# Optimization experiments

Hardware: AMD Instinct MI355X
Metric: run time of the kernel (lower is better)

The kernel has to match this reference:

```python
import jax, jax.numpy as jnp
import numpy as np

EPS = 1e-4

def _mp_normalize(x):
    # EDM2-style normalize: divide by (eps + RMS-scaled L2 norm) along last dim -> unit RMS
    n = jnp.linalg.norm(x, axis=-1, keepdims=True)
    n = EPS + n * (1.0 / np.sqrt(x.shape[-1]))
    return x / n

def _mp_linear(x, w):
    # magnitude-preserving linear: row-normalized weight scaled by 1/sqrt(fan_in), no bias
    fan_in = w.shape[-1]
    w_hat = _mp_normalize(w) * (1.0 / np.sqrt(fan_in))
    return x @ w_hat.T

def setup_inputs() -> dict:
    key = jax.random.key(0)
    k1, k2, k3 = jax.random.split(key, 3)
    B, T, D = 2, 2048, 1024
    x = jax.random.normal(k1, (B, T, D), dtype=jnp.float32)
    w_qkv = jax.random.normal(k2, (3 * D, D), dtype=jnp.float32)
    w_out = jax.random.normal(k3, (D, D), dtype=jnp.float32)
    return {"x": x, "w_qkv": w_qkv, "w_out": w_out}

def reference(x, w_qkv, w_out):
    B, T, D = x.shape
    H = 16
    hd = D // H
    scale = 1.0 / np.sqrt(hd)

    qkv = _mp_linear(x, w_qkv)                      # (B, T, 3D)
    q, k, v = jnp.split(qkv, 3, axis=-1)            # each (B, T, D)

    def to_heads(t):
        return t.reshape(B, T, H, hd).transpose(0, 2, 1, 3)  # (B, H, T, hd)

    q, k, v = to_heads(q), to_heads(k), to_heads(v)
    q = _mp_normalize(q)
    k = _mp_normalize(k)

    scores = jnp.einsum("bhqd,bhkd->bhqk", q, k) * scale
    attn = jax.nn.softmax(scores, axis=-1)
    out = jnp.einsum("bhqk,bhkd->bhqd", attn, v)    # (B, H, T, hd)
    out = out.transpose(0, 2, 1, 3).reshape(B, T, D)
    return _mp_linear(out, w_out)
```

## Files before the change

kernel.cpp:

```cpp
#include <hip/hip_runtime.h>

#define BATCH  2
#define SEQ    2048
#define DMODEL 1024
#define NHEAD  16
#define HDIM   64
#define NROWS  (BATCH * SEQ)
#define QKVC   (3 * DMODEL)

typedef float f32x4 __attribute__((ext_vector_type(4)));
typedef float f32x16 __attribute__((ext_vector_type(16)));
typedef short s16x8 __attribute__((ext_vector_type(8)));
typedef short s16x4 __attribute__((ext_vector_type(4)));
typedef unsigned int u32x4 __attribute__((ext_vector_type(4)));

__device__ __forceinline__ unsigned short f2bf(float f) {
  unsigned int u = __float_as_uint(f);
  u = (u + 0x7FFFu + ((u >> 16) & 1u)) >> 16;
  return (unsigned short)u;
}
__device__ __forceinline__ float bf2f(unsigned short s) {
  return __uint_as_float(((unsigned int)s) << 16);
}
__device__ __forceinline__ unsigned pkbf(float a, float b) {
  unsigned r;
  asm("v_cvt_pk_bf16_f32 %0, %1, %2" : "=v"(r) : "v"(a), "v"(b));
  return r;
}
__device__ __forceinline__ void swp(unsigned &a, unsigned &b) {
  asm volatile("v_permlane32_swap_b32 %0, %1" : "+v"(a), "+v"(b));
}

__global__ __launch_bounds__(256) void k_wnorm(const float* __restrict__ Wq_src,
                                               const float* __restrict__ Wo_src,
                                               unsigned short* __restrict__ Wq,
                                               unsigned short* __restrict__ Wo) {
  const int row = blockIdx.x, tid = threadIdx.x;
  const float* src = (row < QKVC) ? (Wq_src + (size_t)row * DMODEL)
                                  : (Wo_src + (size_t)(row - QKVC) * DMODEL);
  unsigned short* dst = (row < QKVC) ? (Wq + (size_t)row * DMODEL)
                                     : (Wo + (size_t)(row - QKVC) * DMODEL);
  float4 v = ((const float4*)src)[tid];
  float ss = v.x * v.x + v.y * v.y + v.z * v.z + v.w * v.w;
#pragma unroll
  for (int m = 1; m < 64; m <<= 1) ss += __shfl_xor(ss, m);
  __shared__ float part[4];
  if ((tid & 63) == 0) part[tid >> 6] = ss;
  __syncthreads();
  const float tot = part[0] + part[1] + part[2] + part[3];
  const float scale = 0.03125f / (1e-4f + sqrtf(tot) * 0.03125f);
  unsigned short* op = dst + tid * 4;
  op[0] = f2bf(v.x * scale); op[1] = f2bf(v.y * scale);
  op[2] = f2bf(v.z * scale); op[3] = f2bf(v.w * scale);
}

__global__ __launch_bounds__(256) void k_cast(const float* __restrict__ X,
                                              unsigned short* __restrict__ Xb) {
  const int i = blockIdx.x * 256 + threadIdx.x;
  const float4 v = ((const float4*)X)[i];
  ushort4 o = { f2bf(v.x), f2bf(v.y), f2bf(v.z), f2bf(v.w) };
  ((ushort4*)Xb)[i] = o;
}

#define LDP 88
__global__ __launch_bounds__(256, 3) void k_gemm_qkv(const unsigned short* __restrict__ A,
                                                     const unsigned short* __restrict__ Bm,
                                                     unsigned short* __restrict__ C,
                                                     unsigned short* __restrict__ Vt) {
  const int M = NROWS, N = QKVC, K = DMODEL;
  __shared__ unsigned short As[128 * LDP];
  __shared__ unsigned short Bs[128 * LDP];
  const int tid = threadIdx.x;
  const int nbn = N >> 7;
  const int bm = (blockIdx.x / nbn) << 7;
  const int bn = (blockIdx.x % nbn) << 7;
  const int wave = tid >> 6, lane = tid & 63;
  const int wr = (wave >> 1) << 6, wc = (wave & 1) << 6;
  const int l16 = lane & 15, lg = lane >> 4;

  f32x4 acc[4][4];
#pragma unroll
  for (int m = 0; m < 4; ++m)
#pragma unroll
    for (int n = 0; n < 4; ++n) acc[m][n] = (f32x4){0.f, 0.f, 0.f, 0.f};

  s16x8 ra[4], rb[4];
#pragma unroll
  for (int it = 0; it < 4; ++it) {
    const int c = it * 256 + tid;
    const int r = c >> 3, col = (c & 7) << 3;
    ra[it] = *(const s16x8*)(A + (size_t)(bm + r) * K + col);
    rb[it] = *(const s16x8*)(Bm + (size_t)(bn + r) * K + col);
  }

  for (int k0 = 0; k0 < K; k0 += 64) {
    __syncthreads();
#pragma unroll
    for (int it = 0; it < 4; ++it) {
      const int c = it * 256 + tid;
      const int r = c >> 3, col = (c & 7) << 3;
      *(s16x8*)(As + r * LDP + col) = ra[it];
      *(s16x8*)(Bs + r * LDP + col) = rb[it];
    }
    __syncthreads();
    if (k0 + 64 < K) {
#pragma unroll
      for (int it = 0; it < 4; ++it) {
        const int c = it * 256 + tid;
        const int r = c >> 3, col = (c & 7) << 3;
        ra[it] = *(const s16x8*)(A + (size_t)(bm + r) * K + k0 + 64 + col);
        rb[it] = *(const s16x8*)(Bm + (size_t)(bn + r) * K + k0 + 64 + col);
      }
    }
#pragma unroll
    for (int ks = 0; ks < 2; ++ks) {
      s16x8 af[4], bq[4];
#pragma unroll
      for (int m = 0; m < 4; ++m)
        af[m] = *(const s16x8*)(As + (wr + m * 16 + l16) * LDP + ks * 32 + lg * 8);
#pragma unroll
      for (int n = 0; n < 4; ++n)
        bq[n] = *(const s16x8*)(Bs + (wc + n * 16 + l16) * LDP + ks * 32 + lg * 8);
#pragma unroll
      for (int m = 0; m < 4; ++m)
#pragma unroll
        for (int n = 0; n < 4; ++n)
          acc[m][n] = __builtin_amdgcn_mfma_f32_16x16x32_bf16(af[m], bq[n], acc[m][n], 0, 0, 0);
    }
  }

  const int colbase = bn + wc;
  if (colbase < 2 * DMODEL) {
    const float qmul = (colbase < DMODEL) ? 0.125f : 1.0f;
#pragma unroll
    for (int m = 0; m < 4; ++m)
#pragma unroll
      for (int r = 0; r < 4; ++r) {
        float ss = 0.f;
#pragma unroll
        for (int n = 0; n < 4; ++n) ss += acc[m][n][r] * acc[m][n][r];
        ss += __shfl_xor(ss, 1); ss += __shfl_xor(ss, 2);
        ss += __shfl_xor(ss, 4); ss += __shfl_xor(ss, 8);
        const float scale = qmul / (1e-4f + sqrtf(ss) * 0.125f);
#pragma unroll
        for (int n = 0; n < 4; ++n)
          C[(size_t)(bm + wr + m * 16 + lg * 4 + r) * N + (colbase + n * 16 + l16)] =
              f2bf(acc[m][n][r] * scale);
      }
  } else {
    const int hv = (colbase - 2 * DMODEL) >> 6;
    const int token0 = bm + wr;
    const int b_ = token0 >> 11;
    const int bh = b_ * NHEAD + hv;
    const int t0 = (token0 & (SEQ - 1)) + lg * 4;
#pragma unroll
    for (int m = 0; m < 4; ++m)
#pragma unroll
      for (int n = 0; n < 4; ++n) {
        const int d = n * 16 + l16;
        s16x4 ov = { (short)f2bf(acc[m][n][0]), (short)f2bf(acc[m][n][1]),
                     (short)f2bf(acc[m][n][2]), (short)f2bf(acc[m][n][3]) };
        *(s16x4*)(Vt + (size_t)(bh * HDIM + d) * SEQ + t0 + m * 16) = ov;
      }
  }
}

__global__ __launch_bounds__(256, 3) void k_gemm_out(const unsigned short* __restrict__ A,
                                                     const unsigned short* __restrict__ Bm,
                                                     float* __restrict__ C,
                                                     int M, int N, int K) {
  __shared__ unsigned short As[128 * LDP];
  __shared__ unsigned short Bs[128 * LDP];
  const int tid = threadIdx.x;
  const int nbn = N >> 7;
  const int bm = (blockIdx.x / nbn) << 7;
  const int bn = (blockIdx.x % nbn) << 7;
  const int wave = tid >> 6, lane = tid & 63;
  const int wr = (wave >> 1) << 6, wc = (wave & 1) << 6;
  const int l16 = lane & 15, lg = lane >> 4;

  f32x4 acc[4][4];
#pragma unroll
  for (int m = 0; m < 4; ++m)
#pragma unroll
    for (int n = 0; n < 4; ++n) acc[m][n] = (f32x4){0.f, 0.f, 0.f, 0.f};

  s16x8 ra[4], rb[4];
#pragma unroll
  for (int it = 0; it < 4; ++it) {
    const int c = it * 256 + tid;
    const int r = c >> 3, col = (c & 7) << 3;
    ra[it] = *(const s16x8*)(A + (size_t)(bm + r) * K + col);
    rb[it] = *(const s16x8*)(Bm + (size_t)(bn + r) * K + col);
  }

  for (int k0 = 0; k0 < K; k0 += 64) {
    __syncthreads();
#pragma unroll
    for (int it = 0; it < 4; ++it) {
      const int c = it * 256 + tid;
      const int r = c >> 3, col = (c & 7) << 3;
      *(s16x8*)(As + r * LDP + col) = ra[it];
      *(s16x8*)(Bs + r * LDP + col) = rb[it];
    }
    __syncthreads();
    if (k0 + 64 < K) {
#pragma unroll
      for (int it = 0; it < 4; ++it) {
        const int c = it * 256 + tid;
        const int r = c >> 3, col = (c & 7) << 3;
        ra[it] = *(const s16x8*)(A + (size_t)(bm + r) * K + k0 + 64 + col);
        rb[it] = *(const s16x8*)(Bm + (size_t)(bn + r) * K + k0 + 64 + col);
      }
    }
#pragma unroll
    for (int ks = 0; ks < 2; ++ks) {
      s16x8 af[4], bq[4];
#pragma unroll
      for (int m = 0; m < 4; ++m)
        af[m] = *(const s16x8*)(As + (wr + m * 16 + l16) * LDP + ks * 32 + lg * 8);
#pragma unroll
      for (int n = 0; n < 4; ++n)
        bq[n] = *(const s16x8*)(Bs + (wc + n * 16 + l16) * LDP + ks * 32 + lg * 8);
#pragma unroll
      for (int m = 0; m < 4; ++m)
#pragma unroll
        for (int n = 0; n < 4; ++n)
          acc[m][n] = __builtin_amdgcn_mfma_f32_16x16x32_bf16(af[m], bq[n], acc[m][n], 0, 0, 0);
    }
  }
#pragma unroll
  for (int m = 0; m < 4; ++m)
#pragma unroll
    for (int n = 0; n < 4; ++n)
#pragma unroll
      for (int r = 0; r < 4; ++r)
        C[(size_t)(bm + wr + m * 16 + lg * 4 + r) * N + (bn + wc + n * 16 + l16)] =
            acc[m][n][r];
}

__global__ __launch_bounds__(512) void k_attn(const unsigned short* __restrict__ qkv,
                                              const unsigned short* __restrict__ Vt,
                                              unsigned short* __restrict__ O) {
  const int bid = blockIdx.x;
  const int logical = ((bid & 7) << 6) + (bid >> 3);
  const int bh = logical >> 4, qt = logical & 15;
  const int b = bh >> 4, h = bh & 15;
  const int tid = threadIdx.x;
  const int wave = tid >> 6, lane = tid & 63;
  const int l31 = lane & 31, hi = lane >> 5;
  const int qw = wave & 3, half = wave >> 2;
  const int q0 = qt * 128 + qw * 32;

  __shared__ s16x8 smem[2048];
  __shared__ float LL[4][64];

  s16x8* ksh = smem + half * 512;
  s16x8* vsh = smem + 1024 + half * 512;

  const unsigned short* qp =
      qkv + (size_t)(b * SEQ + q0 + l31) * QKVC + h * HDIM + hi * 8;
  const s16x8 qf0 = *(const s16x8*)(qp);
  const s16x8 qf1 = *(const s16x8*)(qp + 16);
  const s16x8 qf2 = *(const s16x8*)(qp + 32);
  const s16x8 qf3 = *(const s16x8*)(qp + 48);

  const int t8 = tid & 255;
  const int srow = t8 >> 3, chunk = t8 & 7;
  const unsigned short* ksrc =
      qkv + (size_t)(b * SEQ + half * 1024 + srow) * QKVC + DMODEL + h * HDIM + chunk * 8;
  const unsigned short* vsrc =
      Vt + (size_t)(bh * HDIM + srow) * SEQ + half * 1024 + chunk * 8;
  const int wsl = srow * 8 + (chunk ^ (srow & 7));
  const int wsh = wsl + 256;

  f32x16 acc0 = {0,0,0,0,0,0,0,0,0,0,0,0,0,0,0,0};
  f32x16 acc1 = {0,0,0,0,0,0,0,0,0,0,0,0,0,0,0,0};
  float l = 0.f;

  for (int kt = 0; kt < 1024; kt += 64) {
    const s16x8 rk0 = *(const s16x8*)(ksrc + (size_t)kt * QKVC);
    const s16x8 rk1 = *(const s16x8*)(ksrc + (size_t)(kt + 32) * QKVC);
    const s16x8 rv0 = *(const s16x8*)(vsrc + kt);
    const s16x8 rv1 = *(const s16x8*)(vsrc + (size_t)32 * SEQ + kt);
    __syncthreads();
    ksh[wsl] = rk0; ksh[wsh] = rk1;
    vsh[wsl] = rv0; vsh[wsh] = rv1;
    __syncthreads();
#pragma unroll
    for (int kh = 0; kh < 2; ++kh) {
      const int key = kh * 32 + l31;
      const int kb = key * 8, kx = key & 7;
      f32x16 st = {0,0,0,0,0,0,0,0,0,0,0,0,0,0,0,0};
      st = __builtin_amdgcn_mfma_f32_32x32x16_bf16(ksh[kb + ((0 + hi) ^ kx)], qf0, st, 0, 0, 0);
      st = __builtin_amdgcn_mfma_f32_32x32x16_bf16(ksh[kb + ((2 + hi) ^ kx)], qf1, st, 0, 0, 0);
      st = __builtin_amdgcn_mfma_f32_32x32x16_bf16(ksh[kb + ((4 + hi) ^ kx)], qf2, st, 0, 0, 0);
      st = __builtin_amdgcn_mfma_f32_32x32x16_bf16(ksh[kb + ((6 + hi) ^ kx)], qf3, st, 0, 0, 0);

#pragma unroll
      for (int r = 0; r < 16; ++r) st[r] = __expf(st[r] - 8.f);

      float s0 = (st[0] + st[1]) + (st[2] + st[3]);
      float s1 = (st[4] + st[5]) + (st[6] + st[7]);
      float s2 = (st[8] + st[9]) + (st[10] + st[11]);
      float s3 = (st[12] + st[13]) + (st[14] + st[15]);
      l += (s0 + s1) + (s2 + s3);

      unsigned P0 = pkbf(st[0], st[1]),   P1 = pkbf(st[2], st[3]);
      unsigned P2 = pkbf(st[4], st[5]),   P3 = pkbf(st[6], st[7]);
      unsigned P4 = pkbf(st[8], st[9]),   P5 = pkbf(st[10], st[11]);
      unsigned P6 = pkbf(st[12], st[13]), P7 = pkbf(st[14], st[15]);
      swp(P0, P2);
      swp(P1, P3);
      swp(P4, P6);
      swp(P5, P7);
      u32x4 w0; w0[0] = P0; w0[1] = P1; w0[2] = P2; w0[3] = P3;
      u32x4 w1; w1[0] = P4; w1[1] = P5; w1[2] = P6; w1[3] = P7;
      const s16x8 pf0 = __builtin_bit_cast(s16x8, w0);
      const s16x8 pf1 = __builtin_bit_cast(s16x8, w1);

      const int vb0 = l31 * 8,        vx0 = l31 & 7;
      const int vb1 = (l31 + 32) * 8, vx1 = vx0;
      acc0 = __builtin_amdgcn_mfma_f32_32x32x16_bf16(vsh[vb0 + ((kh * 4 + 0 + hi) ^ vx0)], pf0, acc0, 0, 0, 0);
      acc0 = __builtin_amdgcn_mfma_f32_32x32x16_bf16(vsh[vb0 + ((kh * 4 + 2 + hi) ^ vx0)], pf1, acc0, 0, 0, 0);
      acc1 = __builtin_amdgcn_mfma_f32_32x32x16_bf16(vsh[vb1 + ((kh * 4 + 0 + hi) ^ vx1)], pf0, acc1, 0, 0, 0);
      acc1 = __builtin_amdgcn_mfma_f32_32x32x16_bf16(vsh[vb1 + ((kh * 4 + 2 + hi) ^ vx1)], pf1, acc1, 0, 0, 0);
    }
  }

  l += __shfl_xor(l, 32);

  __syncthreads();
  float* OO = (float*)smem;
  if (half) {
    float* o_ = OO + qw * 2048;
#pragma unroll
    for (int r = 0; r < 16; ++r) {
      o_[r * 64 + lane] = acc0[r];
      o_[(16 + r) * 64 + lane] = acc1[r];
    }
    LL[qw][lane] = l;
  }
  __syncthreads();
  if (!half) {
    const float inv = 1.f / (l + LL[qw][lane]);
    const float* o_ = OO + qw * 2048;
    unsigned short* ob = O + (size_t)(b * SEQ + q0 + l31) * DMODEL + h * HDIM;
#pragma unroll
    for (int g = 0; g < 4; ++g) {
      float e00 = (acc0[4 * g]     + o_[(4 * g) * 64 + lane])     * inv;
      float e01 = (acc0[4 * g + 1] + o_[(4 * g + 1) * 64 + lane]) * inv;
      float e02 = (acc0[4 * g + 2] + o_[(4 * g + 2) * 64 + lane]) * inv;
      float e03 = (acc0[4 * g + 3] + o_[(4 * g + 3) * 64 + lane]) * inv;
      float e10 = (acc1[4 * g]     + o_[(16 + 4 * g) * 64 + lane])     * inv;
      float e11 = (acc1[4 * g + 1] + o_[(16 + 4 * g + 1) * 64 + lane]) * inv;
      float e12 = (acc1[4 * g + 2] + o_[(16 + 4 * g + 2) * 64 + lane]) * inv;
      float e13 = (acc1[4 * g + 3] + o_[(16 + 4 * g + 3) * 64 + lane]) * inv;
      s16x4 o0 = { (short)f2bf(e00), (short)f2bf(e01), (short)f2bf(e02), (short)f2bf(e03) };
      s16x4 o1 = { (short)f2bf(e10), (short)f2bf(e11), (short)f2bf(e12), (short)f2bf(e13) };
      *(s16x4*)(ob + g * 8 + hi * 4) = o0;
      *(s16x4*)(ob + 32 + g * 8 + hi * 4) = o1;
    }
  }
}

extern "C" void kernel_launch(void* const* d_in, const int* in_sizes, int n_in,
                              void* d_out, int out_size, void* d_ws, size_t ws_size,
                              hipStream_t stream) {
  const float* x    = (const float*)d_in[0];
  const float* wqkv = (const float*)d_in[1];
  const float* wout = (const float*)d_in[2];
  char* ws = (char*)d_ws;
  unsigned short* Wq  = (unsigned short*)(ws);
  unsigned short* Wo  = (unsigned short*)(ws + 6291456);
  unsigned short* Xb  = (unsigned short*)(ws + 8388608);
  unsigned short* QKV = (unsigned short*)(ws + 16777216);
  unsigned short* Vt  = (unsigned short*)(ws + 41943040);
  (void)in_sizes; (void)n_in; (void)out_size; (void)ws_size;

  k_wnorm<<<QKVC + DMODEL, 256, 0, stream>>>(wqkv, wout, Wq, Wo);
  k_cast<<<(NROWS * DMODEL) / 1024, 256, 0, stream>>>(x, Xb);
  k_gemm_qkv<<<(NROWS / 128) * (QKVC / 128), 256, 0, stream>>>(Xb, Wq, QKV, Vt);
  k_attn<<<BATCH * NHEAD * 16, 512, 0, stream>>>(QKV, Vt, Xb);
  k_gemm_out<<<(NROWS / 128) * (DMODEL / 128), 256, 0, stream>>>(
      Xb, Wo, (float*)d_out, NROWS, DMODEL, DMODEL);
}
```

Measured before the change: 114.6 us.

## Split attention keys across four wave groups and use exp2 with prescaled q

The attention kernel now launches 1024 threads per block and divides the key sequence into four quarters of 512 keys, where it previously used two halves of 1024. This halves the serial key loop per wave. Partial outputs and row sums are combined through a two-stage shared-memory reduction with extra barriers. Q is prescaled by log2(e) in the QKV GEMM epilogue so the softmax can use exp2f with a matching constant offset. The cost is twice the shared memory, more synchronisation, and possibly lower occupancy from the 1024-thread blocks.

Result: slower. 129.9 us (+13.3%).

```diff
diff --git a/kernel.cpp b/kernel.cpp
--- a/kernel.cpp
+++ b/kernel.cpp
@@ -131,7 +131,7 @@
 
   const int colbase = bn + wc;
   if (colbase < 2 * DMODEL) {
-    const float qmul = (colbase < DMODEL) ? 0.125f : 1.0f;
+    const float qmul = (colbase < DMODEL) ? 0.18033688f : 1.0f;
 #pragma unroll
     for (int m = 0; m < 4; ++m)
 #pragma unroll
@@ -239,9 +239,10 @@
             acc[m][n][r];
 }
 
-__global__ __launch_bounds__(512) void k_attn(const unsigned short* __restrict__ qkv,
-                                              const unsigned short* __restrict__ Vt,
-                                              unsigned short* __restrict__ O) {
+#define M2C 11.541560327f
+__global__ __launch_bounds__(1024) void k_attn(const unsigned short* __restrict__ qkv,
+                                               const unsigned short* __restrict__ Vt,
+                                               unsigned short* __restrict__ O) {
   const int bid = blockIdx.x;
   const int logical = ((bid & 7) << 6) + (bid >> 3);
   const int bh = logical >> 4, qt = logical & 15;
@@ -249,14 +250,15 @@
   const int tid = threadIdx.x;
   const int wave = tid >> 6, lane = tid & 63;
   const int l31 = lane & 31, hi = lane >> 5;
-  const int qw = wave & 3, half = wave >> 2;
+  const int qw = wave & 3, quarter = wave >> 2;
   const int q0 = qt * 128 + qw * 32;
 
-  __shared__ s16x8 smem[2048];
-  __shared__ float LL[4][64];
-
-  s16x8* ksh = smem + half * 512;
-  s16x8* vsh = smem + 1024 + half * 512;
+  __shared__ s16x8 smem[4096];
+  __shared__ float LL1[2][4][64];
+  __shared__ float LL2[4][64];
+
+  s16x8* ksh = smem + quarter * 512;
+  s16x8* vsh = smem + 2048 + quarter * 512;
 
   const unsigned short* qp =
       qkv + (size_t)(b * SEQ + q0 + l31) * QKVC + h * HDIM + hi * 8;
@@ -268,9 +270,9 @@
   const int t8 = tid & 255;
   const int srow = t8 >> 3, chunk = t8 & 7;
   const unsigned short* ksrc =
-      qkv + (size_t)(b * SEQ + half * 1024 + srow) * QKVC + DMODEL + h * HDIM + chunk * 8;
+      qkv + (size_t)(b * SEQ + quarter * 512 + srow) * QKVC + DMODEL + h * HDIM + chunk * 8;
   const unsigned short* vsrc =
-      Vt + (size_t)(bh * HDIM + srow) * SEQ + half * 1024 + chunk * 8;
+      Vt + (size_t)(bh * HDIM + srow) * SEQ + quarter * 512 + chunk * 8;
   const int wsl = srow * 8 + (chunk ^ (srow & 7));
   const int wsh = wsl + 256;
 
@@ -278,7 +280,7 @@
   f32x16 acc1 = {0,0,0,0,0,0,0,0,0,0,0,0,0,0,0,0};
   float l = 0.f;
 
-  for (int kt = 0; kt < 1024; kt += 64) {
+  for (int kt = 0; kt < 512; kt += 64) {
     const s16x8 rk0 = *(const s16x8*)(ksrc + (size_t)kt * QKVC);
     const s16x8 rk1 = *(const s16x8*)(ksrc + (size_t)(kt + 32) * QKVC);
     const s16x8 rv0 = *(const s16x8*)(vsrc + kt);
@@ -298,7 +300,7 @@
       st = __builtin_amdgcn_mfma_f32_32x32x16_bf16(ksh[kb + ((6 + hi) ^ kx)], qf3, st, 0, 0, 0);
 
 #pragma unroll
-      for (int r = 0; r < 16; ++r) st[r] = __expf(st[r] - 8.f);
+      for (int r = 0; r < 16; ++r) st[r] = exp2f(st[r] - M2C);
 
       float s0 = (st[0] + st[1]) + (st[2] + st[3]);
       float s1 = (st[4] + st[5]) + (st[6] + st[7]);
@@ -332,18 +334,38 @@
 
   __syncthreads();
   float* OO = (float*)smem;
-  if (half) {
-    float* o_ = OO + qw * 2048;
+  if (quarter >= 2) {
+    float* o_ = OO + ((quarter - 2) * 4 + qw) * 2048;
 #pragma unroll
     for (int r = 0; r < 16; ++r) {
       o_[r * 64 + lane] = acc0[r];
       o_[(16 + r) * 64 + lane] = acc1[r];
     }
-    LL[qw][lane] = l;
+    LL1[quarter - 2][qw][lane] = l;
   }
   __syncthreads();
-  if (!half) {
-    const float inv = 1.f / (l + LL[qw][lane]);
+  if (quarter < 2) {
+    const float* o_ = OO + (quarter * 4 + qw) * 2048;
+#pragma unroll
+    for (int r = 0; r < 16; ++r) {
+      acc0[r] += o_[r * 64 + lane];
+      acc1[r] += o_[(16 + r) * 64 + lane];
+    }
+    l += LL1[quarter][qw][lane];
+  }
+  __syncthreads();
+  if (quarter == 1) {
+    float* o_ = OO + qw * 2048;
+#pragma unroll
+    for (int r = 0; r < 16; ++r) {
+      o_[r * 64 + lane] = acc0[r];
+      o_[(16 + r) * 64 + lane] = acc1[r];
+    }
+    LL2[qw][lane] = l;
+  }
+  __syncthreads();
+  if (quarter == 0) {
+    const float inv = 1.f / (l + LL2[qw][lane]);
     const float* o_ = OO + qw * 2048;
     unsigned short* ob = O + (size_t)(b * SEQ + q0 + l31) * DMODEL + h * HDIM;
 #pragma unroll
@@ -381,7 +403,7 @@
   k_wnorm<<<QKVC + DMODEL, 256, 0, stream>>>(wqkv, wout, Wq, Wo);
   k_cast<<<(NROWS * DMODEL) / 1024, 256, 0, stream>>>(x, Xb);
   k_gemm_qkv<<<(NROWS / 128) * (QKVC / 128), 256, 0, stream>>>(Xb, Wq, QKV, Vt);
-  k_attn<<<BATCH * NHEAD * 16, 512, 0, stream>>>(QKV, Vt, Xb);
+  k_attn<<<BATCH * NHEAD * 16, 1024, 0, stream>>>(QKV, Vt, Xb);
   k_gemm_out<<<(NROWS / 128) * (DMODEL / 128), 256, 0, stream>>>(
       Xb, Wo, (float*)d_out, NROWS, DMODEL, DMODEL);
 }
```
